# Optimization experiments

Hardware: AMD Instinct MI355X
Metric: run time of the kernel (lower is better)

## Reference

```python
import jax, jax.numpy as jnp
import numpy as np

B, T, ISIZE = 64, 512, 1024
OSIZE = ISIZE
HSIZE = 4 * OSIZE
LN_EPS = 1e-6  # ieps_ln_default in the source repo


def setup_inputs() -> dict:
    key = jax.random.key(0)
    ks = jax.random.split(key, 7)
    s1 = 1.0 / np.sqrt(ISIZE + OSIZE)
    s2 = 1.0 / np.sqrt(HSIZE)
    return {
        "x": jax.random.normal(ks[0], (B, T, ISIZE), dtype=jnp.float32),
        "W1": jax.random.normal(ks[1], (ISIZE + OSIZE, HSIZE), dtype=jnp.float32) * s1,
        "b1": jnp.zeros((HSIZE,), dtype=jnp.float32),
        "ln_g": jnp.ones((HSIZE,), dtype=jnp.float32),
        "ln_b": jnp.zeros((HSIZE,), dtype=jnp.float32),
        "W2": jax.random.normal(ks[2], (HSIZE, ISIZE), dtype=jnp.float32) * s2,
        "b2": jnp.zeros((ISIZE,), dtype=jnp.float32),
        "init_hx": jnp.zeros((1, OSIZE), dtype=jnp.float32),
    }


def _layernorm(h, g, b):
    mu = jnp.mean(h, axis=-1, keepdims=True)
    var = jnp.mean(jnp.square(h - mu), axis=-1, keepdims=True)
    return (h - mu) * jax.lax.rsqrt(var + LN_EPS) * g + b


def reference(x, W1, b1, ln_g, ln_b, W2, b2, init_hx):
    # x: [B, T, isize]; recurrence hx_{t} = net(cat(x_t, hx_{t-1})) + hx_{t-1}
    hx0 = jnp.broadcast_to(init_hx, (x.shape[0], init_hx.shape[-1]))

    def step(hx, xt):
        h = jnp.concatenate([xt, hx], axis=-1) @ W1 + b1       # [B, hsize]
        h = jax.nn.gelu(_layernorm(h, ln_g, ln_b), approximate=False)
        hx = h @ W2 + b2 + hx                                  # [B, isize]
        return hx, hx

    _, rs = jax.lax.scan(step, hx0, jnp.swapaxes(x, 0, 1))     # [T, B, isize]
    return jnp.swapaxes(rs, 0, 1)                              # [B, T, isize]
```

## Files before the change

### kernel.cpp

```cpp
#include <hip/hip_runtime.h>
#include <hip/hip_bf16.h>
#include <math.h>

typedef __bf16 bf16x8 __attribute__((ext_vector_type(8)));
typedef float f32x4 __attribute__((ext_vector_type(4)));
typedef unsigned long long u64;
typedef u64 u64x2 __attribute__((ext_vector_type(2)));

#define TT 512
#define ISZ 1024
#define HSZ 4096
#define NBLK 256
#define NTHR 512
#define LN_EPS 1e-6f
#define SCOPE_AGENT __HIP_MEMORY_SCOPE_AGENT

union U128 { u64 u[2]; u64x2 p; bf16x8 v; };

__device__ __forceinline__ bf16x8 nt_ld16(const __bf16* p) {
  U128 r;
  r.p = __builtin_nontemporal_load((const u64x2*)p);
  return r.v;
}
__device__ __forceinline__ void coh_st16(__bf16* p, bf16x8 v) {
  U128 r; r.v = v;
  u64* q = (u64*)p;
  __hip_atomic_store(q,     r.u[0], __ATOMIC_RELAXED, SCOPE_AGENT);
  __hip_atomic_store(q + 1, r.u[1], __ATOMIC_RELAXED, SCOPE_AGENT);
}

__device__ __forceinline__ float gelu_f(float v) {
  const float u = v * 0.70710678118654752f;
  const float x = fabsf(u);
  const float t = __builtin_amdgcn_rcpf(fmaf(0.3275911f, x, 1.0f));
  float p = fmaf(1.061405429f, t, -1.453152027f);
  p = fmaf(p, t, 1.421413741f);
  p = fmaf(p, t, -0.284496736f);
  p = fmaf(p, t, 0.254829592f);
  p = p * t;
  const float e = p * __expf(-x * x);
  const float erfv = copysignf(1.0f - e, u);
  return 0.5f * v * (1.0f + erfv);
}

__device__ __forceinline__ int frag_idx(int row, int u) {
  return (((u >> 2) * 4 + (row >> 4)) * 64 + (u & 3) * 16 + (row & 15)) * 8;
}

__global__ void prep_w1(const float* __restrict__ W1, __bf16* __restrict__ w1p) {
  int t = blockIdx.x * blockDim.x + threadIdx.x;
  int k = t >> 9;
  int n8 = (t & 511) << 3;
  const float* src = W1 + (size_t)k * HSZ + n8;
  float4 f0 = *(const float4*)src;
  float4 f1 = *(const float4*)(src + 4);
  int kgrp = k >> 3, kk = k & 7;
  float vals[8] = {f0.x, f0.y, f0.z, f0.w, f1.x, f1.y, f1.z, f1.w};
#pragma unroll
  for (int i = 0; i < 8; ++i) {
    int n = n8 + i;
    int nb = n >> 4, col = n & 15;
    w1p[(size_t)nb * 32768 + kgrp * 128 + col * 8 + kk] = (__bf16)vals[i];
  }
}

__global__ void prep_w2(const float* __restrict__ W2, __bf16* __restrict__ w2p) {
  int t = blockIdx.x * blockDim.x + threadIdx.x;
  int k = t >> 7;
  int n8 = (t & 127) << 3;
  const float* src = W2 + (size_t)k * ISZ + n8;
  float4 f0 = *(const float4*)src;
  float4 f1 = *(const float4*)(src + 4);
  int kgrp = k >> 3, kk = k & 7;
  float vals[8] = {f0.x, f0.y, f0.z, f0.w, f1.x, f1.y, f1.z, f1.w};
#pragma unroll
  for (int i = 0; i < 8; ++i) {
    int n = n8 + i;
    int cg = n >> 4, col = n & 15;
    w2p[(size_t)cg * 65536 + kgrp * 128 + col * 8 + kk] = (__bf16)vals[i];
  }
}

__global__ void prep_x(const float* __restrict__ x, __bf16* __restrict__ xbf) {
  int tid = blockIdx.x * blockDim.x + threadIdx.x;
  int c8 = tid & 127;
  int t = (tid >> 7) & 511;
  int row = tid >> 16;
  const float* src = x + ((size_t)row * TT + t) * ISZ + c8 * 8;
  float4 f0 = *(const float4*)src;
  float4 f1 = *(const float4*)(src + 4);
  float vals[8] = {f0.x, f0.y, f0.z, f0.w, f1.x, f1.y, f1.z, f1.w};
  bf16x8 v;
#pragma unroll
  for (int i = 0; i < 8; ++i) v[i] = (__bf16)vals[i];
  int kh = c8 >> 2, lane = (c8 & 3) * 16 + (row & 15), m = row >> 4;
  *(bf16x8*)&xbf[(size_t)t * 65536 + (((kh * 4 + m) * 64 + lane) << 3)] = v;
}

__global__ void prep_state(const float* __restrict__ init_hx,
                           float* __restrict__ hxf32, __bf16* __restrict__ hxbf,
                           unsigned* __restrict__ syncbuf) {
  int t = blockIdx.x * blockDim.x + threadIdx.x;
  int row = t >> 10, c = t & 1023;
  float v = init_hx[c];
  hxf32[t] = v;
  int kh = c >> 5, l = ((c >> 3) & 3) * 16 + (row & 15), m = row >> 4;
  hxbf[((kh * 4 + m) * 64 + l) * 8 + (c & 7)] = (__bf16)v;
  if (t < 16672) syncbuf[t] = 0u;
}

__device__ __forceinline__ void gbar_arrive(unsigned* __restrict__ arr,
                                            int j, unsigned target) {
  __syncthreads();
  if (threadIdx.x == 0)
    __hip_atomic_store(&arr[j * 32], target, __ATOMIC_RELAXED, SCOPE_AGENT);
}
__device__ __forceinline__ void gbar_wait(unsigned* __restrict__ arr,
                                          unsigned* __restrict__ gflag,
                                          int j, unsigned target) {
  const int tid = threadIdx.x;
  if (j < 8 && tid < 32) {
    const unsigned* p = &arr[(tid * 8 + j) * 32];
    int guard = 0;
    for (;;) {
      unsigned v = __hip_atomic_load(p, __ATOMIC_RELAXED, SCOPE_AGENT);
      if (__all(v >= target)) break;
      if (++guard > (1 << 20)) break;
      __builtin_amdgcn_s_sleep(1);
    }
    asm volatile("" ::: "memory");
    if (tid == 0)
      __hip_atomic_store(&gflag[j * 32], target, __ATOMIC_RELAXED, SCOPE_AGENT);
  }
  if (tid < 8) {
    const unsigned* p = &gflag[tid * 32];
    int guard = 0;
    for (;;) {
      unsigned v = __hip_atomic_load(p, __ATOMIC_RELAXED, SCOPE_AGENT);
      if (__all(v >= target)) break;
      if (++guard > (1 << 20)) break;
      __builtin_amdgcn_s_sleep(1);
    }
  }
  asm volatile("" ::: "memory");
  __syncthreads();
}
__device__ __forceinline__ void gbar(unsigned* __restrict__ arr,
                                     unsigned* __restrict__ gflag,
                                     int j, unsigned target) {
  gbar_arrive(arr, j, target);
  gbar_wait(arr, gflag, j, target);
}

__device__ __forceinline__ void xbar_arrive(unsigned* __restrict__ xarr,
                                            int xk, int xrank, unsigned target) {
  __syncthreads();
  if (threadIdx.x == 0)
    __hip_atomic_store(&xarr[(xk * 32 + xrank) * 32], target, __ATOMIC_RELAXED, SCOPE_AGENT);
}
__device__ __forceinline__ void xbar_wait(unsigned* __restrict__ xarr,
                                          int xk, unsigned target) {
  const int tid = threadIdx.x;
  if (tid < 32) {
    const unsigned* p = &xarr[(xk * 32 + tid) * 32];
    int guard = 0;
    for (;;) {
      unsigned v = __hip_atomic_load(p, __ATOMIC_RELAXED, SCOPE_AGENT);
      if (__all(v >= target)) break;
      if (++guard > (1 << 20)) break;
      __builtin_amdgcn_s_sleep(1);
    }
  }
  asm volatile("" ::: "memory");
  __syncthreads();
}

template <bool USE_XBF>
__global__ __launch_bounds__(NTHR, 1) void rnn_persist(
    const float* __restrict__ x, const float* __restrict__ b1,
    const float* __restrict__ ln_g, const float* __restrict__ ln_b,
    const float* __restrict__ b2, float* __restrict__ out,
    const __bf16* __restrict__ w1p, const __bf16* __restrict__ w2p,
    const __bf16* __restrict__ xbf,
    __bf16* __restrict__ hbf, __bf16* __restrict__ abf,
    __bf16* __restrict__ ablocal, __bf16* __restrict__ hxbf,
    float* __restrict__ hxf32, unsigned* __restrict__ arr,
    unsigned* __restrict__ gflag, unsigned* __restrict__ xarr,
    unsigned* __restrict__ ticket)
{
  __shared__ __bf16 w1s[32768];
  __shared__ float red[8192];
  __shared__ __bf16 abuf[1024];
  __shared__ int sh_meta[4];

  const int j = blockIdx.x;
  const int tid = threadIdx.x;
  const int w = tid >> 6;
  const int l = tid & 63;
  const int l4 = l >> 4, l15 = l & 15;

  if (tid == 0) {
    unsigned xcd = ((unsigned)__builtin_amdgcn_s_getreg(63508)) & 7u;
    unsigned r = __hip_atomic_fetch_add(&ticket[xcd], 1u, __ATOMIC_RELAXED, SCOPE_AGENT);
    sh_meta[0] = (int)xcd;
    sh_meta[1] = (int)r;
  }

  {
    const bf16x8* src = (const bf16x8*)(w1p + (size_t)j * 32768);
    bf16x8* dst = (bf16x8*)w1s;
#pragma unroll
    for (int i = 0; i < 8; ++i) dst[tid + i * 512] = src[tid + i * 512];
  }

  unsigned tc = 1;
  gbar(arr, gflag, j, tc);

  if (tid == 0) {
    int ok = 1;
#pragma unroll
    for (int i = 0; i < 8; ++i)
      ok &= (__hip_atomic_load(&ticket[i], __ATOMIC_RELAXED, SCOPE_AGENT) == 32u);
    sh_meta[2] = ok && (sh_meta[1] < 32);
  }
  __syncthreads();
  const int xk = sh_meta[0];
  const int xrank = sh_meta[1];
  const bool lmode = (sh_meta[2] != 0);
  __bf16* abl = ablocal + (size_t)xk * 262144;

  const float b1v = b1[j * 16 + l15];
  const int g = j >> 6, cg = j & 63;
  const float b2v = b2[cg * 16 + l15];

  const int prodj = ((l >> 3) & 3) * 64 + w * 8 + (l & 7);

  for (int t = 0; t < TT; ++t) {
    f32x4 hac[4];
#pragma unroll
    for (int m = 0; m < 4; ++m) hac[m] = (f32x4){0.f, 0.f, 0.f, 0.f};
#pragma unroll
    for (int i = 0; i < 4; ++i) {
      const int ks = w * 4 + i;
      bf16x8 bfr = *(const bf16x8*)&w1s[((4 * ks + l4) * 16 + l15) * 8];
      if (USE_XBF) {
        const __bf16* xb = xbf + (size_t)t * 65536 + (size_t)ks * 2048;
#pragma unroll
        for (int m = 0; m < 4; ++m) {
          bf16x8 af = *(const bf16x8*)&xb[(m * 64 + l) * 8];
          hac[m] = __builtin_amdgcn_mfma_f32_16x16x32_bf16(af, bfr, hac[m], 0, 0, 0);
        }
      } else {
        const int k = ks * 32 + l4 * 8;
#pragma unroll
        for (int m = 0; m < 4; ++m) {
          const int row = m * 16 + l15;
          const float* p = x + ((size_t)row * TT + t) * ISZ + k;
          float4 f0 = *(const float4*)p;
          float4 f1 = *(const float4*)(p + 4);
          bf16x8 af;
          af[0] = (__bf16)f0.x; af[1] = (__bf16)f0.y;
          af[2] = (__bf16)f0.z; af[3] = (__bf16)f0.w;
          af[4] = (__bf16)f1.x; af[5] = (__bf16)f1.y;
          af[6] = (__bf16)f1.z; af[7] = (__bf16)f1.w;
          hac[m] = __builtin_amdgcn_mfma_f32_16x16x32_bf16(af, bfr, hac[m], 0, 0, 0);
        }
      }
    }
    {
      const unsigned* p = &arr[prodj * 32];
      int guard = 0;
      for (;;) {
        unsigned v = __hip_atomic_load(p, __ATOMIC_RELAXED, SCOPE_AGENT);
        if (__all(v >= tc)) break;
        if (++guard > (1 << 20)) break;
        __builtin_amdgcn_s_sleep(1);
      }
      asm volatile("" ::: "memory");
    }

#pragma unroll
    for (int i = 0; i < 4; ++i) {
      const int kh = w * 4 + i;
      bf16x8 bfr = *(const bf16x8*)&w1s[((4 * (32 + kh) + l4) * 16 + l15) * 8];
#pragma unroll
      for (int m = 0; m < 4; ++m) {
        bf16x8 af = nt_ld16(&hxbf[((kh * 4 + m) * 64 + l) * 8]);
        hac[m] = __builtin_amdgcn_mfma_f32_16x16x32_bf16(af, bfr, hac[m], 0, 0, 0);
      }
    }
#pragma unroll
    for (int m = 0; m < 4; ++m)
      *(f32x4*)&red[((w * 4 + m) * 64 + l) * 4] = hac[m];
    __syncthreads();
    if (w < 4) {
      f32x4 h = *(const f32x4*)&red[((0 * 4 + w) * 64 + l) * 4];
#pragma unroll
      for (int s = 1; s < 8; ++s)
        h += *(const f32x4*)&red[((s * 4 + w) * 64 + l) * 4];
#pragma unroll
      for (int r = 0; r < 4; ++r)
        abuf[(w * 16 + l4 * 4 + r) * 16 + l15] = (__bf16)(h[r] + b1v);
    }
    __syncthreads();
    if (tid < 128) {
      const int m = tid >> 5, q2s = (tid >> 4) & 1, rr = tid & 15;
      bf16x8 vv = *(const bf16x8*)&abuf[(m * 16 + rr) * 16 + q2s * 8];
      const int k2 = j >> 1, q2 = (j & 1) * 2 + q2s;
      coh_st16(&hbf[(((k2 * 4 + m) * 64) + q2 * 16 + rr) * 8], vv);
    }
    ++tc; gbar(arr, gflag, j, tc);

    if (lmode) {
      const int u = tid;
      const int R0 = xrank * 2, R1 = R0 + 1;
      const int i0 = frag_idx(R0, u), i1 = frag_idx(R1, u);
      bf16x8 h0 = nt_ld16(hbf + i0);
      bf16x8 h1 = nt_ld16(hbf + i1);
      float s0 = 0.f, q0 = 0.f, s1 = 0.f, q1 = 0.f;
#pragma unroll
      for (int e = 0; e < 8; ++e) {
        float v0 = (float)h0[e], v1 = (float)h1[e];
        s0 += v0; q0 += v0 * v0; s1 += v1; q1 += v1 * v1;
      }
#pragma unroll
      for (int m = 1; m < 64; m <<= 1) {
        s0 += __shfl_xor(s0, m, 64); q0 += __shfl_xor(q0, m, 64);
        s1 += __shfl_xor(s1, m, 64); q1 += __shfl_xor(q1, m, 64);
      }
      if (l == 0) *(f32x4*)&red[4096 + w * 4] = (f32x4){s0, q0, s1, q1};
      __syncthreads();
      float S0 = 0.f, Q0 = 0.f, S1 = 0.f, Q1 = 0.f;
#pragma unroll
      for (int w2 = 0; w2 < 8; ++w2) {
        f32x4 p = *(const f32x4*)&red[4096 + w2 * 4];
        S0 += p[0]; Q0 += p[1]; S1 += p[2]; Q1 += p[3];
      }
      const float mu0 = S0 * (1.f / 4096.f), mu1 = S1 * (1.f / 4096.f);
      const float rs0 = rsqrtf(Q0 * (1.f / 4096.f) - mu0 * mu0 + LN_EPS);
      const float rs1 = rsqrtf(Q1 * (1.f / 4096.f) - mu1 * mu1 + LN_EPS);
      const int c0 = (u >> 2) * 32 + (u & 3) * 8;
      float4 ga = *(const float4*)(ln_g + c0), gb = *(const float4*)(ln_g + c0 + 4);
      float4 ea = *(const float4*)(ln_b + c0), eb = *(const float4*)(ln_b + c0 + 4);
      float gk[8] = {ga.x, ga.y, ga.z, ga.w, gb.x, gb.y, gb.z, gb.w};
      float ek[8] = {ea.x, ea.y, ea.z, ea.w, eb.x, eb.y, eb.z, eb.w};
      bf16x8 a0, a1;
#pragma unroll
      for (int e = 0; e < 8; ++e) {
        a0[e] = (__bf16)gelu_f(((float)h0[e] - mu0) * rs0 * gk[e] + ek[e]);
        a1[e] = (__bf16)gelu_f(((float)h1[e] - mu1) * rs1 * gk[e] + ek[e]);
      }
      *(bf16x8*)(abl + i0) = a0;
      *(bf16x8*)(abl + i1) = a1;
    } else {
      const int u = tid;
      const int R = j >> 2, q = j & 3;
      const int iR = frag_idx(R, u);
      bf16x8 hv = nt_ld16(hbf + iR);
      float s0 = 0.f, q0 = 0.f;
#pragma unroll
      for (int e = 0; e < 8; ++e) { float v = (float)hv[e]; s0 += v; q0 += v * v; }
#pragma unroll
      for (int m = 1; m < 64; m <<= 1) {
        s0 += __shfl_xor(s0, m, 64); q0 += __shfl_xor(q0, m, 64);
      }
      if (l == 0) { red[4096 + w * 2] = s0; red[4096 + w * 2 + 1] = q0; }
      __syncthreads();
      float S = 0.f, Q = 0.f;
#pragma unroll
      for (int w2 = 0; w2 < 8; ++w2) { S += red[4096 + w2 * 2]; Q += red[4096 + w2 * 2 + 1]; }
      const float mu = S * (1.f / 4096.f);
      const float rs = rsqrtf(Q * (1.f / 4096.f) - mu * mu + LN_EPS);
      if ((tid >> 7) == q) {
        const int c0 = (u >> 2) * 32 + (u & 3) * 8;
        float4 ga = *(const float4*)(ln_g + c0), gb = *(const float4*)(ln_g + c0 + 4);
        float4 ea = *(const float4*)(ln_b + c0), eb = *(const float4*)(ln_b + c0 + 4);
        float gk[8] = {ga.x, ga.y, ga.z, ga.w, gb.x, gb.y, gb.z, gb.w};
        float ek[8] = {ea.x, ea.y, ea.z, ea.w, eb.x, eb.y, eb.z, eb.w};
        bf16x8 av;
#pragma unroll
        for (int e = 0; e < 8; ++e)
          av[e] = (__bf16)gelu_f(((float)hv[e] - mu) * rs * gk[e] + ek[e]);
        coh_st16(abf + iR, av);
      }
    }

    ++tc;
    if (lmode) xbar_arrive(xarr, xk, xrank, tc);
    else       gbar_arrive(arr, j, tc);
    bf16x8 wreg[16];
#pragma unroll
    for (int i = 0; i < 16; ++i)
      wreg[i] = *(const bf16x8*)&w2p[((size_t)cg * 512 + (w * 16 + i) * 4 + l4) * 128 + l15 * 8];
    if (lmode) xbar_wait(xarr, xk, tc);
    else       gbar_wait(arr, gflag, j, tc);

    {
      f32x4 cac = {0.f, 0.f, 0.f, 0.f};
      if (lmode) {
#pragma unroll
        for (int i = 0; i < 16; ++i) {
          const int s2 = w * 16 + i;
          bf16x8 af = *(const bf16x8*)&abl[((s2 * 4 + g) * 64 + l) * 8];
          cac = __builtin_amdgcn_mfma_f32_16x16x32_bf16(af, wreg[i], cac, 0, 0, 0);
        }
      } else {
#pragma unroll
        for (int i = 0; i < 16; ++i) {
          const int s2 = w * 16 + i;
          bf16x8 af = nt_ld16(&abf[((s2 * 4 + g) * 64 + l) * 8]);
          cac = __builtin_amdgcn_mfma_f32_16x16x32_bf16(af, wreg[i], cac, 0, 0, 0);
        }
      }
      *(f32x4*)&red[(w * 64 + l) * 4] = cac;
    }
    __syncthreads();
    if (w < 4) {
      float s = 0.f;
#pragma unroll
      for (int w2 = 0; w2 < 8; ++w2) s += red[(w2 * 64 + l) * 4 + w];
      const int row = g * 16 + l4 * 4 + w;
      const int c = cg * 16 + l15;
      const float vNew = s + b2v + hxf32[row * ISZ + c];
      hxf32[row * ISZ + c] = vNew;
      out[((size_t)row * TT + t) * ISZ + c] = vNew;
      const int kh = c >> 5, lh = ((c >> 3) & 3) * 16 + (row & 15), mh = row >> 4;
      union { __bf16 b; unsigned short s16; } cv; cv.b = (__bf16)vNew;
      __hip_atomic_store((unsigned short*)&hxbf[((kh * 4 + mh) * 64 + lh) * 8 + (c & 7)],
                         cv.s16, __ATOMIC_RELAXED, SCOPE_AGENT);
    }
    ++tc; gbar_arrive(arr, j, tc);
  }
}

extern "C" void kernel_launch(void* const* d_in, const int* in_sizes, int n_in,
                              void* d_out, int out_size, void* d_ws, size_t ws_size,
                              hipStream_t stream) {
  const float* x       = (const float*)d_in[0];
  const float* W1      = (const float*)d_in[1];
  const float* b1      = (const float*)d_in[2];
  const float* ln_g    = (const float*)d_in[3];
  const float* ln_b    = (const float*)d_in[4];
  const float* W2      = (const float*)d_in[5];
  const float* b2      = (const float*)d_in[6];
  const float* init_hx = (const float*)d_in[7];
  float* out = (float*)d_out;

  char* ws = (char*)d_ws;
  __bf16* w1p     = (__bf16*)(ws);
  __bf16* w2p     = (__bf16*)(ws + 16777216ull);
  __bf16* hbf     = (__bf16*)(ws + 25165824ull);
  __bf16* abf     = (__bf16*)(ws + 25690112ull);
  __bf16* ablocal = (__bf16*)(ws + 26214400ull);
  __bf16* hxbf    = (__bf16*)(ws + 30408704ull);
  float* hxf32    = (float*)(ws + 30539776ull);
  unsigned* arr   = (unsigned*)(ws + 30801920ull);
  unsigned* gflag = (unsigned*)(ws + 30834688ull);
  unsigned* xarr  = (unsigned*)(ws + 30835712ull);
  unsigned* ticket= (unsigned*)(ws + 30868480ull);
  __bf16* xbf     = (__bf16*)(ws + 33554432ull);
  const bool use_xbf = (ws_size >= 33554432ull + 67108864ull);

  prep_w1<<<4096, 256, 0, stream>>>(W1, w1p);
  prep_w2<<<2048, 256, 0, stream>>>(W2, w2p);
  prep_state<<<256, 256, 0, stream>>>(init_hx, hxf32, hxbf, arr);
  if (use_xbf) {
    prep_x<<<16384, 256, 0, stream>>>(x, xbf);
    rnn_persist<true><<<NBLK, NTHR, 0, stream>>>(
        x, b1, ln_g, ln_b, b2, out, w1p, w2p, xbf, hbf, abf, ablocal,
        hxbf, hxf32, arr, gflag, xarr, ticket);
  } else {
    rnn_persist<false><<<NBLK, NTHR, 0, stream>>>(
        x, b1, ln_g, ln_b, b2, out, w1p, w2p, xbf, hbf, abf, ablocal,
        hxbf, hxf32, arr, gflag, xarr, ticket);
  }
}
```

Baseline: 8.550 ms.

## Overlap next-step x-projection MFMA with grid barrier wait and hoist LN params

The x-part of the first GEMM for step t+1 is computed between arriving at and waiting on the grid barrier after the h store, so it hides barrier latency instead of running at the start of each step. The barrier wait becomes a flat poll where 64 threads each check four arrival counters. LayerNorm gamma and beta are loaded once into registers before the loop. This raises register pressure (hacx carried across iterations plus gk/ek) and changes the barrier wait pattern.

```diff
diff --git a/kernel.cpp b/kernel.cpp
--- a/kernel.cpp
+++ b/kernel.cpp
@@ -150,6 +150,30 @@
                                      int j, unsigned target) {
   gbar_arrive(arr, j, target);
   gbar_wait(arr, gflag, j, target);
+}
+
+__device__ __forceinline__ void flat_wait(const unsigned* __restrict__ arr,
+                                          unsigned target) {
+  const int tid = threadIdx.x;
+  if (tid < 64) {
+    const unsigned* p0 = &arr[(tid * 4 + 0) * 32];
+    const unsigned* p1 = &arr[(tid * 4 + 1) * 32];
+    const unsigned* p2 = &arr[(tid * 4 + 2) * 32];
+    const unsigned* p3 = &arr[(tid * 4 + 3) * 32];
+    int guard = 0;
+    for (;;) {
+      unsigned v0 = __hip_atomic_load(p0, __ATOMIC_RELAXED, SCOPE_AGENT);
+      unsigned v1 = __hip_atomic_load(p1, __ATOMIC_RELAXED, SCOPE_AGENT);
+      unsigned v2 = __hip_atomic_load(p2, __ATOMIC_RELAXED, SCOPE_AGENT);
+      unsigned v3 = __hip_atomic_load(p3, __ATOMIC_RELAXED, SCOPE_AGENT);
+      int ok = (v0 >= target) & (v1 >= target) & (v2 >= target) & (v3 >= target);
+      if (__all(ok)) break;
+      if (++guard > (1 << 20)) break;
+      __builtin_amdgcn_s_sleep(1);
+    }
+  }
+  asm volatile("" ::: "memory");
+  __syncthreads();
 }
 
 __device__ __forceinline__ void xbar_arrive(unsigned* __restrict__ xarr,
@@ -235,8 +259,18 @@
 
   const int prodj = ((l >> 3) & 3) * 64 + w * 8 + (l & 7);
 
-  for (int t = 0; t < TT; ++t) {
-    f32x4 hac[4];
+  const int c0 = (tid >> 2) * 32 + (tid & 3) * 8;
+  float gk[8], ek[8];
+  {
+    float4 ga = *(const float4*)(ln_g + c0), gb = *(const float4*)(ln_g + c0 + 4);
+    float4 ea = *(const float4*)(ln_b + c0), eb = *(const float4*)(ln_b + c0 + 4);
+    gk[0] = ga.x; gk[1] = ga.y; gk[2] = ga.z; gk[3] = ga.w;
+    gk[4] = gb.x; gk[5] = gb.y; gk[6] = gb.z; gk[7] = gb.w;
+    ek[0] = ea.x; ek[1] = ea.y; ek[2] = ea.z; ek[3] = ea.w;
+    ek[4] = eb.x; ek[5] = eb.y; ek[6] = eb.z; ek[7] = eb.w;
+  }
+
+  auto do_xhalf = [&](int tt, f32x4* hac) {
 #pragma unroll
     for (int m = 0; m < 4; ++m) hac[m] = (f32x4){0.f, 0.f, 0.f, 0.f};
 #pragma unroll
@@ -244,7 +278,7 @@
       const int ks = w * 4 + i;
       bf16x8 bfr = *(const bf16x8*)&w1s[((4 * ks + l4) * 16 + l15) * 8];
       if (USE_XBF) {
-        const __bf16* xb = xbf + (size_t)t * 65536 + (size_t)ks * 2048;
+        const __bf16* xb = xbf + (size_t)tt * 65536 + (size_t)ks * 2048;
 #pragma unroll
         for (int m = 0; m < 4; ++m) {
           bf16x8 af = *(const bf16x8*)&xb[(m * 64 + l) * 8];
@@ -255,7 +289,7 @@
 #pragma unroll
         for (int m = 0; m < 4; ++m) {
           const int row = m * 16 + l15;
-          const float* p = x + ((size_t)row * TT + t) * ISZ + k;
+          const float* p = x + ((size_t)row * TT + tt) * ISZ + k;
           float4 f0 = *(const float4*)p;
           float4 f1 = *(const float4*)(p + 4);
           bf16x8 af;
@@ -267,6 +301,12 @@
         }
       }
     }
+  };
+
+  f32x4 hacx[4];
+  do_xhalf(0, hacx);
+
+  for (int t = 0; t < TT; ++t) {
     {
       const unsigned* p = &arr[prodj * 32];
       int guard = 0;
@@ -286,12 +326,12 @@
 #pragma unroll
       for (int m = 0; m < 4; ++m) {
         bf16x8 af = nt_ld16(&hxbf[((kh * 4 + m) * 64 + l) * 8]);
-        hac[m] = __builtin_amdgcn_mfma_f32_16x16x32_bf16(af, bfr, hac[m], 0, 0, 0);
+        hacx[m] = __builtin_amdgcn_mfma_f32_16x16x32_bf16(af, bfr, hacx[m], 0, 0, 0);
       }
     }
 #pragma unroll
     for (int m = 0; m < 4; ++m)
-      *(f32x4*)&red[((w * 4 + m) * 64 + l) * 4] = hac[m];
+      *(f32x4*)&red[((w * 4 + m) * 64 + l) * 4] = hacx[m];
     __syncthreads();
     if (w < 4) {
       f32x4 h = *(const f32x4*)&red[((0 * 4 + w) * 64 + l) * 4];
@@ -309,7 +349,10 @@
       const int k2 = j >> 1, q2 = (j & 1) * 2 + q2s;
       coh_st16(&hbf[(((k2 * 4 + m) * 64) + q2 * 16 + rr) * 8], vv);
     }
-    ++tc; gbar(arr, gflag, j, tc);
+    ++tc;
+    gbar_arrive(arr, j, tc);
+    if (t + 1 < TT) do_xhalf(t + 1, hacx);
+    flat_wait(arr, tc);
 
     if (lmode) {
       const int u = tid;
@@ -339,11 +382,6 @@
       const float mu0 = S0 * (1.f / 4096.f), mu1 = S1 * (1.f / 4096.f);
       const float rs0 = rsqrtf(Q0 * (1.f / 4096.f) - mu0 * mu0 + LN_EPS);
       const float rs1 = rsqrtf(Q1 * (1.f / 4096.f) - mu1 * mu1 + LN_EPS);
-      const int c0 = (u >> 2) * 32 + (u & 3) * 8;
-      float4 ga = *(const float4*)(ln_g + c0), gb = *(const float4*)(ln_g + c0 + 4);
-      float4 ea = *(const float4*)(ln_b + c0), eb = *(const float4*)(ln_b + c0 + 4);
-      float gk[8] = {ga.x, ga.y, ga.z, ga.w, gb.x, gb.y, gb.z, gb.w};
-      float ek[8] = {ea.x, ea.y, ea.z, ea.w, eb.x, eb.y, eb.z, eb.w};
       bf16x8 a0, a1;
 #pragma unroll
       for (int e = 0; e < 8; ++e) {
@@ -372,11 +410,6 @@
       const float mu = S * (1.f / 4096.f);
       const float rs = rsqrtf(Q * (1.f / 4096.f) - mu * mu + LN_EPS);
       if ((tid >> 7) == q) {
-        const int c0 = (u >> 2) * 32 + (u & 3) * 8;
-        float4 ga = *(const float4*)(ln_g + c0), gb = *(const float4*)(ln_g + c0 + 4);
-        float4 ea = *(const float4*)(ln_b + c0), eb = *(const float4*)(ln_b + c0 + 4);
-        float gk[8] = {ga.x, ga.y, ga.z, ga.w, gb.x, gb.y, gb.z, gb.w};
-        float ek[8] = {ea.x, ea.y, ea.z, ea.w, eb.x, eb.y, eb.z, eb.w};
         bf16x8 av;
 #pragma unroll
         for (int e = 0; e < 8; ++e)
```

Measured after the change: 9.470 ms. 10.8% more time.

## Stage hidden state into per-XCD local copy before recurrent matmul

Applied to the files above, without the earlier changes.

When blocks are evenly mapped to XCDs (lmode), each block waits only on the few producers it is responsible for. It copies its slice of the bf16 hidden state into a per-XCD replica, then synchronizes within the XCD and reads the replica for the recurrent half of the first GEMM. This is meant to replace 256 blocks polling many global flags and reading hx across dies with traffic that stays local to each XCD's cache. In exchange it adds an extra XCD barrier and a copy per timestep, and it shifts the tc counter increments, which must stay consistent with the later barriers.

```diff
diff --git a/kernel.cpp b/kernel.cpp
--- a/kernel.cpp
+++ b/kernel.cpp
@@ -183,7 +183,8 @@
     const __bf16* __restrict__ w1p, const __bf16* __restrict__ w2p,
     const __bf16* __restrict__ xbf,
     __bf16* __restrict__ hbf, __bf16* __restrict__ abf,
-    __bf16* __restrict__ ablocal, __bf16* __restrict__ hxbf,
+    __bf16* __restrict__ ablocal, __bf16* __restrict__ hxlocal,
+    __bf16* __restrict__ hxbf,
     float* __restrict__ hxf32, unsigned* __restrict__ arr,
     unsigned* __restrict__ gflag, unsigned* __restrict__ xarr,
     unsigned* __restrict__ ticket)
@@ -228,15 +229,16 @@
   const int xrank = sh_meta[1];
   const bool lmode = (sh_meta[2] != 0);
   __bf16* abl = ablocal + (size_t)xk * 262144;
+  __bf16* hxl = hxlocal + (size_t)xk * 65536;
 
   const float b1v = b1[j * 16 + l15];
   const int g = j >> 6, cg = j & 63;
   const float b2v = b2[cg * 16 + l15];
 
   const int prodj = ((l >> 3) & 3) * 64 + w * 8 + (l & 7);
-
-  for (int t = 0; t < TT; ++t) {
-    f32x4 hac[4];
+  const int stgj = ((tid >> 1) & 3) * 64 + 2 * xrank + (tid & 1);
+
+  auto do_xhalf = [&](int tt, f32x4* hac) {
 #pragma unroll
     for (int m = 0; m < 4; ++m) hac[m] = (f32x4){0.f, 0.f, 0.f, 0.f};
 #pragma unroll
@@ -244,7 +246,7 @@
       const int ks = w * 4 + i;
       bf16x8 bfr = *(const bf16x8*)&w1s[((4 * ks + l4) * 16 + l15) * 8];
       if (USE_XBF) {
-        const __bf16* xb = xbf + (size_t)t * 65536 + (size_t)ks * 2048;
+        const __bf16* xb = xbf + (size_t)tt * 65536 + (size_t)ks * 2048;
 #pragma unroll
         for (int m = 0; m < 4; ++m) {
           bf16x8 af = *(const bf16x8*)&xb[(m * 64 + l) * 8];
@@ -255,7 +257,7 @@
 #pragma unroll
         for (int m = 0; m < 4; ++m) {
           const int row = m * 16 + l15;
-          const float* p = x + ((size_t)row * TT + t) * ISZ + k;
+          const float* p = x + ((size_t)row * TT + tt) * ISZ + k;
           float4 f0 = *(const float4*)p;
           float4 f1 = *(const float4*)(p + 4);
           bf16x8 af;
@@ -267,28 +269,68 @@
         }
       }
     }
-    {
-      const unsigned* p = &arr[prodj * 32];
-      int guard = 0;
-      for (;;) {
-        unsigned v = __hip_atomic_load(p, __ATOMIC_RELAXED, SCOPE_AGENT);
-        if (__all(v >= tc)) break;
-        if (++guard > (1 << 20)) break;
-        __builtin_amdgcn_s_sleep(1);
+  };
+
+  for (int t = 0; t < TT; ++t) {
+    f32x4 hac[4];
+    if (lmode) {
+      if (tid < 8) {
+        const unsigned* p = &arr[stgj * 32];
+        int guard = 0;
+        for (;;) {
+          unsigned v = __hip_atomic_load(p, __ATOMIC_RELAXED, SCOPE_AGENT);
+          if (__all(v >= tc)) break;
+          if (++guard > (1 << 20)) break;
+          __builtin_amdgcn_s_sleep(1);
+        }
       }
       asm volatile("" ::: "memory");
-    }
-
-#pragma unroll
-    for (int i = 0; i < 4; ++i) {
-      const int kh = w * 4 + i;
-      bf16x8 bfr = *(const bf16x8*)&w1s[((4 * (32 + kh) + l4) * 16 + l15) * 8];
-#pragma unroll
-      for (int m = 0; m < 4; ++m) {
-        bf16x8 af = nt_ld16(&hxbf[((kh * 4 + m) * 64 + l) * 8]);
-        hac[m] = __builtin_amdgcn_mfma_f32_16x16x32_bf16(af, bfr, hac[m], 0, 0, 0);
-      }
-    }
+      __syncthreads();
+      if (tid < 256) {
+        const int off = xrank * 2048 + tid * 8;
+        bf16x8 v = nt_ld16(hxbf + off);
+        *(bf16x8*)(hxl + off) = v;
+      }
+      ++tc; xbar_arrive(xarr, xk, xrank, tc);
+      do_xhalf(t, hac);
+      xbar_wait(xarr, xk, tc);
+
+#pragma unroll
+      for (int i = 0; i < 4; ++i) {
+        const int kh = w * 4 + i;
+        bf16x8 bfr = *(const bf16x8*)&w1s[((4 * (32 + kh) + l4) * 16 + l15) * 8];
+#pragma unroll
+        for (int m = 0; m < 4; ++m) {
+          bf16x8 af = *(const bf16x8*)&hxl[((kh * 4 + m) * 64 + l) * 8];
+          hac[m] = __builtin_amdgcn_mfma_f32_16x16x32_bf16(af, bfr, hac[m], 0, 0, 0);
+        }
+      }
+    } else {
+      do_xhalf(t, hac);
+      {
+        const unsigned* p = &arr[prodj * 32];
+        int guard = 0;
+        for (;;) {
+          unsigned v = __hip_atomic_load(p, __ATOMIC_RELAXED, SCOPE_AGENT);
+          if (__all(v >= tc)) break;
+          if (++guard > (1 << 20)) break;
+          __builtin_amdgcn_s_sleep(1);
+        }
+        asm volatile("" ::: "memory");
+      }
+      ++tc;
+#pragma unroll
+      for (int i = 0; i < 4; ++i) {
+        const int kh = w * 4 + i;
+        bf16x8 bfr = *(const bf16x8*)&w1s[((4 * (32 + kh) + l4) * 16 + l15) * 8];
+#pragma unroll
+        for (int m = 0; m < 4; ++m) {
+          bf16x8 af = nt_ld16(&hxbf[((kh * 4 + m) * 64 + l) * 8]);
+          hac[m] = __builtin_amdgcn_mfma_f32_16x16x32_bf16(af, bfr, hac[m], 0, 0, 0);
+        }
+      }
+    }
+
 #pragma unroll
     for (int m = 0; m < 4; ++m)
       *(f32x4*)&red[((w * 4 + m) * 64 + l) * 4] = hac[m];
@@ -458,6 +500,7 @@
   unsigned* gflag = (unsigned*)(ws + 30834688ull);
   unsigned* xarr  = (unsigned*)(ws + 30835712ull);
   unsigned* ticket= (unsigned*)(ws + 30868480ull);
+  __bf16* hxlocal = (__bf16*)(ws + 31457280ull);
   __bf16* xbf     = (__bf16*)(ws + 33554432ull);
   const bool use_xbf = (ws_size >= 33554432ull + 67108864ull);
 
@@ -468,10 +511,10 @@
     prep_x<<<16384, 256, 0, stream>>>(x, xbf);
     rnn_persist<true><<<NBLK, NTHR, 0, stream>>>(
         x, b1, ln_g, ln_b, b2, out, w1p, w2p, xbf, hbf, abf, ablocal,
-        hxbf, hxf32, arr, gflag, xarr, ticket);
+        hxlocal, hxbf, hxf32, arr, gflag, xarr, ticket);
   } else {
     rnn_persist<false><<<NBLK, NTHR, 0, stream>>>(
         x, b1, ln_g, ln_b, b2, out, w1p, w2p, xbf, hbf, abf, ablocal,
-        hxbf, hxf32, arr, gflag, xarr, ticket);
-  }
-}
+        hxlocal, hxbf, hxf32, arr, gflag, xarr, ticket);
+  }
+}
```

Result: faster. 8.286 ms (-3.1%).
